# Performance work log

Hardware: AMD Instinct MI355X
Metric: run time of the kernel (lower is better)

## Reference

```python
import jax, jax.numpy as jnp
import numpy as np

RADIUS = 0.1
MAX_GRID_DIM = 96
MAX_COLLISIONS = 128
INCLUDE_SELF = True


def setup_inputs() -> dict:
    key = jax.random.key(0)
    k1, k2, k3 = jax.random.split(key, 3)
    B, N, M, D, C = 2, 8192, 8192, 3, 64
    locs = jax.random.uniform(k1, (B, N, D), dtype=jnp.float32)
    data = jax.random.normal(k2, (B, N, C), dtype=jnp.float32)
    qlocs = jax.random.uniform(k3, (B, M, D), dtype=jnp.float32)
    return {"locs": locs, "data": data, "qlocs": qlocs}


def _hashgrid_order(locs):
    """Returns idxs [B,N] int32 sorting particles by flattened hash-grid cell id.
       idxs[b,i] = original index of the particle at new position i."""
    lower = jnp.min(locs, axis=1, keepdims=True)          # [B,1,D]
    upper = jnp.max(locs, axis=1, keepdims=True)          # [B,1,D]
    # grid dims per batch/dim, cell width = radius, capped at max_grid_dim
    gd = jnp.clip(jnp.floor((upper - lower) / RADIUS).astype(jnp.int32) + 1,
                  1, MAX_GRID_DIM)                        # [B,1,D]
    cell = jnp.floor((locs - lower) / RADIUS).astype(jnp.int32)
    cell = jnp.clip(cell, 0, gd - 1)                      # [B,N,D]
    # mixed-radix flatten: stride[d] = prod(gd[d+1:])
    strides = jnp.concatenate(
        [jnp.cumprod(gd[..., ::-1], axis=-1)[..., ::-1][..., 1:],
         jnp.ones_like(gd[..., :1])], axis=-1)            # [B,1,D]
    cid = jnp.sum(cell * strides, axis=-1)                # [B,N]
    return jnp.argsort(cid, axis=1, stable=True).astype(jnp.int32)


def _collisions(qlocs, nlocs):
    """For each query, indices into reordered locs within RADIUS, lowest-index
       first, padded with -1 up to MAX_COLLISIONS. Returns [B,M,K] int32."""
    B, N, _ = nlocs.shape
    d2 = jnp.sum((qlocs[:, :, None, :] - nlocs[:, None, :, :]) ** 2, axis=-1)  # [B,M,N]
    mask = d2 <= RADIUS * RADIUS
    if not INCLUDE_SELF:
        mask = mask & (d2 > 0)
    # key = particle index if neighbor else N (sentinel); first K after sort
    key = jnp.where(mask, jnp.arange(N, dtype=jnp.int32)[None, None, :], N)
    first_k = jnp.sort(key, axis=-1)[..., :MAX_COLLISIONS]                     # [B,M,K]
    return jnp.where(first_k < N, first_k, -1).astype(jnp.int32)


def reference(locs, data, qlocs):
    idxs = _hashgrid_order(locs)                              # [B,N]
    nlocs = jnp.take_along_axis(locs, idxs[..., None], axis=1)   # reordered locs
    ndata = jnp.take_along_axis(data, idxs[..., None], axis=1)   # reordered data
    neighbors = _collisions(qlocs, nlocs)                     # [B,M,K]
    return nlocs, ndata, idxs, neighbors
```

## Files before the change

### kernel.cpp

```cpp
#include <hip/hip_runtime.h>
#include <cfloat>
#include <math.h>

#define BB 2
#define NN 8192
#define MM 8192
#define CC 64
#define RAD 0.1f
#define R2 0.01f
#define MAXK 128
#define CELL_CAP 4096
#define CS_STRIDE 4100

#define WS_HDR 0
#define WS_SIDX 32
#define WS_CS (WS_SIDX + BB*NN)
#define WS_NL4 (WS_CS + BB*CS_STRIDE)

__device__ __forceinline__ int cell_of(float v, float lo, int g) {
    int c = (int)floorf(__fdiv_rn(v - lo, RAD));
    return min(max(c, 0), g - 1);
}

__global__ __launch_bounds__(1024) void build_kernel(const float* __restrict__ locs,
                                                     int* __restrict__ ws,
                                                     float* __restrict__ idxs_out) {
    const int b = blockIdx.x;
    const int t = threadIdx.x;
    __shared__ int sh[4097 + 1024 + NN];
    int* s_start = sh;
    int* s_aux   = sh + 4097;
    int* s_tmp   = sh + 4097 + 1024;
    float* s_red = (float*)s_tmp;
    __shared__ float s_lo[3];
    __shared__ int   s_g[3];
    __shared__ int   s_str[2];

    const float* L = locs + (size_t)b * NN * 3;

    float mn0 = FLT_MAX, mn1 = FLT_MAX, mn2 = FLT_MAX;
    float mx0 = -FLT_MAX, mx1 = -FLT_MAX, mx2 = -FLT_MAX;
    for (int i = t; i < NN; i += 1024) {
        float x = L[i*3+0], y = L[i*3+1], z = L[i*3+2];
        mn0 = fminf(mn0, x); mx0 = fmaxf(mx0, x);
        mn1 = fminf(mn1, y); mx1 = fmaxf(mx1, y);
        mn2 = fminf(mn2, z); mx2 = fmaxf(mx2, z);
    }
    s_red[t] = mn0; s_red[1024+t] = mn1; s_red[2048+t] = mn2;
    s_red[3072+t] = mx0; s_red[4096+t] = mx1; s_red[5120+t] = mx2;
    __syncthreads();
    for (int s = 512; s > 0; s >>= 1) {
        if (t < s) {
            s_red[t]      = fminf(s_red[t],      s_red[t+s]);
            s_red[1024+t] = fminf(s_red[1024+t], s_red[1024+t+s]);
            s_red[2048+t] = fminf(s_red[2048+t], s_red[2048+t+s]);
            s_red[3072+t] = fmaxf(s_red[3072+t], s_red[3072+t+s]);
            s_red[4096+t] = fmaxf(s_red[4096+t], s_red[4096+t+s]);
            s_red[5120+t] = fmaxf(s_red[5120+t], s_red[5120+t+s]);
        }
        __syncthreads();
    }
    if (t == 0) {
        float lo0 = s_red[0], lo1 = s_red[1024], lo2 = s_red[2048];
        float up0 = s_red[3072], up1 = s_red[4096], up2 = s_red[5120];
        int g0 = min(max((int)floorf(__fdiv_rn(up0 - lo0, RAD)) + 1, 1), 96);
        int g1 = min(max((int)floorf(__fdiv_rn(up1 - lo1, RAD)) + 1, 1), 96);
        int g2 = min(max((int)floorf(__fdiv_rn(up2 - lo2, RAD)) + 1, 1), 96);
        s_lo[0] = lo0; s_lo[1] = lo1; s_lo[2] = lo2;
        s_g[0] = g0; s_g[1] = g1; s_g[2] = g2;
        s_str[0] = g1 * g2; s_str[1] = g2;
        int* hdr = ws + WS_HDR + b * 16;
        hdr[0] = __float_as_int(lo0); hdr[1] = __float_as_int(lo1); hdr[2] = __float_as_int(lo2);
        hdr[3] = g0; hdr[4] = g1; hdr[5] = g2;
        hdr[6] = g1 * g2; hdr[7] = g2; hdr[8] = g0 * g1 * g2;
    }
    __syncthreads();
    const float lo0 = s_lo[0], lo1 = s_lo[1], lo2f = s_lo[2];
    const int g0 = s_g[0], g1 = s_g[1], g2 = s_g[2];
    const int st0 = s_str[0], st1 = s_str[1];
    const int ncells = g0 * g1 * g2;

    for (int c = t; c < CELL_CAP + 1; c += 1024) s_start[c] = 0;
    __syncthreads();

    for (int i = t; i < NN; i += 1024) {
        int c0 = cell_of(L[i*3+0], lo0, g0);
        int c1 = cell_of(L[i*3+1], lo1, g1);
        int c2 = cell_of(L[i*3+2], lo2f, g2);
        atomicAdd(&s_start[c0*st0 + c1*st1 + c2], 1);
    }
    __syncthreads();

    int base4 = t * 4;
    int sum = s_start[base4] + s_start[base4+1] + s_start[base4+2] + s_start[base4+3];
    s_aux[t] = sum;
    __syncthreads();
    for (int off = 1; off < 1024; off <<= 1) {
        int v = (t >= off) ? s_aux[t - off] : 0;
        __syncthreads();
        s_aux[t] += v;
        __syncthreads();
    }
    int run = s_aux[t] - sum;
    for (int k = 0; k < 4; ++k) {
        int cv = s_start[base4 + k];
        s_start[base4 + k] = run;
        run += cv;
    }
    if (t == 1023) s_start[CELL_CAP] = run;
    __syncthreads();

    for (int i = t; i < NN; i += 1024) {
        int c0 = cell_of(L[i*3+0], lo0, g0);
        int c1 = cell_of(L[i*3+1], lo1, g1);
        int c2 = cell_of(L[i*3+2], lo2f, g2);
        int cid = c0*st0 + c1*st1 + c2;
        int pos = atomicAdd(&s_start[cid], 1);
        s_tmp[pos] = i;
    }
    __syncthreads();

    int* cs = ws + WS_CS + b * CS_STRIDE;
    for (int c = t; c <= ncells; c += 1024) cs[c] = (c == 0) ? 0 : s_start[c - 1];

    int* sIdx = ws + WS_SIDX + b * NN;
    for (int p = t; p < NN; p += 1024) {
        int i = s_tmp[p];
        int c0 = cell_of(L[i*3+0], lo0, g0);
        int c1 = cell_of(L[i*3+1], lo1, g1);
        int c2 = cell_of(L[i*3+2], lo2f, g2);
        int cid = c0*st0 + c1*st1 + c2;
        int segs = (cid == 0) ? 0 : s_start[cid - 1];
        int sege = s_start[cid];
        int rank = 0;
        for (int q = segs; q < sege; ++q) rank += (s_tmp[q] < i) ? 1 : 0;
        int f = segs + rank;
        sIdx[f] = i;
        idxs_out[b * NN + f] = (float)i;
    }
}

__global__ __launch_bounds__(256) void reorder_kernel(const float* __restrict__ locs,
                                                      const float* __restrict__ data,
                                                      const int* __restrict__ ws,
                                                      float* __restrict__ nlocs_out,
                                                      float* __restrict__ ndata_out,
                                                      float* __restrict__ nlocs4) {
    int tid = blockIdx.x * 256 + threadIdx.x;
    int b = tid >> 19;
    int r = tid & ((NN * CC) - 1);
    int p = r >> 6;
    int c = r & 63;
    int idx = ws[WS_SIDX + b * NN + p];
    ndata_out[tid] = data[((size_t)b * NN + idx) * CC + c];
    if (c < 3) {
        float v = locs[((size_t)b * NN + idx) * 3 + c];
        nlocs_out[((size_t)b * NN + p) * 3 + c] = v;
        nlocs4[((size_t)b * NN + p) * 4 + c] = v;
    } else if (c == 3) {
        nlocs4[((size_t)b * NN + p) * 4 + 3] = 0.0f;
    }
}

__global__ __launch_bounds__(256) void neigh_kernel(const float* __restrict__ qlocs,
                                                    const float4* __restrict__ P4,
                                                    const int* __restrict__ ws,
                                                    float* __restrict__ neigh_out) {
    const int tid  = blockIdx.x * 256 + threadIdx.x;
    const int q    = tid >> 3;
    const int lane = threadIdx.x & 63;
    const int sub  = lane >> 3;
    const int lg   = lane & 7;
    const int b    = q >> 13;

    const int* hdr = ws + WS_HDR + b * 16;
    float lo0 = __int_as_float(hdr[0]);
    float lo1 = __int_as_float(hdr[1]);
    float lo2f = __int_as_float(hdr[2]);
    int g0 = hdr[3], g1 = hdr[4], g2 = hdr[5];
    int st0 = hdr[6], st1 = hdr[7];
    const int* cs = ws + WS_CS + b * CS_STRIDE;
    const float4* P = P4 + (size_t)b * NN;

    float qx = qlocs[(size_t)q * 3 + 0];
    float qy = qlocs[(size_t)q * 3 + 1];
    float qz = qlocs[(size_t)q * 3 + 2];

    int c0 = (int)floorf(__fdiv_rn(qx - lo0, RAD));
    int c1 = (int)floorf(__fdiv_rn(qy - lo1, RAD));
    int c2 = (int)floorf(__fdiv_rn(qz - lo2f, RAD));
    int a0lo = max(c0 - 1, 0), a0hi = min(c0 + 1, g0 - 1);
    int a1lo = max(c1 - 1, 0), a1hi = min(c1 + 1, g1 - 1);
    int a2lo = max(c2 - 1, 0), a2hi = min(c2 + 1, g2 - 1);

    int cnt = 0;
    float* o = neigh_out + (size_t)q * MAXK;

    if (a0hi >= a0lo && a1hi >= a1lo && a2hi >= a2lo) {
        for (int a0 = a0lo; a0 <= a0hi && cnt < MAXK; ++a0) {
            for (int a1 = a1lo; a1 <= a1hi && cnt < MAXK; ++a1) {
                int basec = a0 * st0 + a1 * st1;
                int ps = cs[basec + a2lo];
                int pe = cs[basec + a2hi + 1];
                for (int base = ps; base < pe && cnt < MAXK; base += 8) {
                    int p = base + lg;
                    bool hit = false;
                    if (p < pe) {
                        float4 v = P[p];
                        float dx = qx - v.x;
                        float dy = qy - v.y;
                        float dz = qz - v.z;
                        float d2 = __fadd_rn(__fadd_rn(__fmul_rn(dx, dx), __fmul_rn(dy, dy)),
                                             __fmul_rn(dz, dz));
                        hit = (d2 <= R2);
                    }
                    unsigned long long m = __ballot(hit);
                    unsigned mb = (unsigned)((m >> (sub * 8)) & 0xFFull);
                    if (hit) {
                        int slot = cnt + __popc(mb & ((1u << lg) - 1u));
                        if (slot < MAXK) o[slot] = (float)p;
                    }
                    cnt += __popc(mb);
                }
            }
        }
    }
    for (int s = cnt + lg; s < MAXK; s += 8) o[s] = -1.0f;
}

extern "C" void kernel_launch(void* const* d_in, const int* in_sizes, int n_in,
                              void* d_out, int out_size, void* d_ws, size_t ws_size,
                              hipStream_t stream) {
    (void)in_sizes; (void)n_in; (void)out_size; (void)ws_size;
    const float* locs  = (const float*)d_in[0];
    const float* data  = (const float*)d_in[1];
    const float* qlocs = (const float*)d_in[2];
    float* out = (float*)d_out;
    float* nlocs_out = out;
    float* ndata_out = out + BB * NN * 3;
    float* idxs_out  = out + BB * NN * 3 + BB * NN * CC;
    float* neigh_out = idxs_out + BB * NN;
    int* wsi = (int*)d_ws;
    float* nlocs4 = (float*)(wsi + WS_NL4);

    build_kernel<<<BB, 1024, 0, stream>>>(locs, wsi, idxs_out);
    reorder_kernel<<<(BB * NN * CC) / 256, 256, 0, stream>>>(locs, data, wsi,
                                                             nlocs_out, ndata_out, nlocs4);
    neigh_kernel<<<(BB * MM * 8) / 256, 256, 0, stream>>>(qlocs, (const float4*)nlocs4, wsi, neigh_out);
}
```

Baseline: 106.8 us.

## Use wave shuffles in build reductions, cache cell ids, widen neighbor query groups

The build kernel now does its min/max reduction and prefix scan with wavefront shuffles instead of long shared-memory tree loops full of block barriers. It also caches each particle's cell id in shared memory so later passes skip recomputing cells from global locs. The neighbor kernel assigns 16 lanes per query instead of 8, preloads all nine cell ranges up front, and drops the early-exit checks on the count. Without those checks, queries that have already filled MAXK slots keep scanning the remaining cells, and each query now occupies twice as many threads.

```diff
diff --git a/kernel.cpp b/kernel.cpp
--- a/kernel.cpp
+++ b/kernel.cpp
@@ -27,11 +27,13 @@
                                                      float* __restrict__ idxs_out) {
     const int b = blockIdx.x;
     const int t = threadIdx.x;
-    __shared__ int sh[4097 + 1024 + NN];
-    int* s_start = sh;
-    int* s_aux   = sh + 4097;
-    int* s_tmp   = sh + 4097 + 1024;
-    float* s_red = (float*)s_tmp;
+    const int lane = t & 63;
+    const int wid = t >> 6;
+    __shared__ int s_start[CELL_CAP + 1];
+    __shared__ int s_aux[16];
+    __shared__ int s_tmp[NN];
+    __shared__ int s_cid[NN];
+    __shared__ float s_red6[16 * 6];
     __shared__ float s_lo[3];
     __shared__ int   s_g[3];
     __shared__ int   s_str[2];
@@ -46,23 +48,30 @@
         mn1 = fminf(mn1, y); mx1 = fmaxf(mx1, y);
         mn2 = fminf(mn2, z); mx2 = fmaxf(mx2, z);
     }
-    s_red[t] = mn0; s_red[1024+t] = mn1; s_red[2048+t] = mn2;
-    s_red[3072+t] = mx0; s_red[4096+t] = mx1; s_red[5120+t] = mx2;
-    __syncthreads();
-    for (int s = 512; s > 0; s >>= 1) {
-        if (t < s) {
-            s_red[t]      = fminf(s_red[t],      s_red[t+s]);
-            s_red[1024+t] = fminf(s_red[1024+t], s_red[1024+t+s]);
-            s_red[2048+t] = fminf(s_red[2048+t], s_red[2048+t+s]);
-            s_red[3072+t] = fmaxf(s_red[3072+t], s_red[3072+t+s]);
-            s_red[4096+t] = fmaxf(s_red[4096+t], s_red[4096+t+s]);
-            s_red[5120+t] = fmaxf(s_red[5120+t], s_red[5120+t+s]);
-        }
-        __syncthreads();
-    }
+    #pragma unroll
+    for (int d = 1; d < 64; d <<= 1) {
+        mn0 = fminf(mn0, __shfl_xor(mn0, d, 64));
+        mn1 = fminf(mn1, __shfl_xor(mn1, d, 64));
+        mn2 = fminf(mn2, __shfl_xor(mn2, d, 64));
+        mx0 = fmaxf(mx0, __shfl_xor(mx0, d, 64));
+        mx1 = fmaxf(mx1, __shfl_xor(mx1, d, 64));
+        mx2 = fmaxf(mx2, __shfl_xor(mx2, d, 64));
+    }
+    if (lane == 0) {
+        s_red6[wid*6+0] = mn0; s_red6[wid*6+1] = mn1; s_red6[wid*6+2] = mn2;
+        s_red6[wid*6+3] = mx0; s_red6[wid*6+4] = mx1; s_red6[wid*6+5] = mx2;
+    }
+    for (int c = t; c < CELL_CAP + 1; c += 1024) s_start[c] = 0;
+    __syncthreads();
     if (t == 0) {
-        float lo0 = s_red[0], lo1 = s_red[1024], lo2 = s_red[2048];
-        float up0 = s_red[3072], up1 = s_red[4096], up2 = s_red[5120];
+        float lo0 = FLT_MAX, lo1 = FLT_MAX, lo2 = FLT_MAX;
+        float up0 = -FLT_MAX, up1 = -FLT_MAX, up2 = -FLT_MAX;
+        for (int w = 0; w < 16; ++w) {
+            lo0 = fminf(lo0, s_red6[w*6+0]); lo1 = fminf(lo1, s_red6[w*6+1]);
+            lo2 = fminf(lo2, s_red6[w*6+2]);
+            up0 = fmaxf(up0, s_red6[w*6+3]); up1 = fmaxf(up1, s_red6[w*6+4]);
+            up2 = fmaxf(up2, s_red6[w*6+5]);
+        }
         int g0 = min(max((int)floorf(__fdiv_rn(up0 - lo0, RAD)) + 1, 1), 96);
         int g1 = min(max((int)floorf(__fdiv_rn(up1 - lo1, RAD)) + 1, 1), 96);
         int g2 = min(max((int)floorf(__fdiv_rn(up2 - lo2, RAD)) + 1, 1), 96);
@@ -80,42 +89,48 @@
     const int st0 = s_str[0], st1 = s_str[1];
     const int ncells = g0 * g1 * g2;
 
-    for (int c = t; c < CELL_CAP + 1; c += 1024) s_start[c] = 0;
-    __syncthreads();
-
-    for (int i = t; i < NN; i += 1024) {
-        int c0 = cell_of(L[i*3+0], lo0, g0);
-        int c1 = cell_of(L[i*3+1], lo1, g1);
-        int c2 = cell_of(L[i*3+2], lo2f, g2);
-        atomicAdd(&s_start[c0*st0 + c1*st1 + c2], 1);
-    }
-    __syncthreads();
-
-    int base4 = t * 4;
-    int sum = s_start[base4] + s_start[base4+1] + s_start[base4+2] + s_start[base4+3];
-    s_aux[t] = sum;
-    __syncthreads();
-    for (int off = 1; off < 1024; off <<= 1) {
-        int v = (t >= off) ? s_aux[t - off] : 0;
-        __syncthreads();
-        s_aux[t] += v;
-        __syncthreads();
-    }
-    int run = s_aux[t] - sum;
-    for (int k = 0; k < 4; ++k) {
-        int cv = s_start[base4 + k];
-        s_start[base4 + k] = run;
-        run += cv;
-    }
-    if (t == 1023) s_start[CELL_CAP] = run;
-    __syncthreads();
-
     for (int i = t; i < NN; i += 1024) {
         int c0 = cell_of(L[i*3+0], lo0, g0);
         int c1 = cell_of(L[i*3+1], lo1, g1);
         int c2 = cell_of(L[i*3+2], lo2f, g2);
         int cid = c0*st0 + c1*st1 + c2;
-        int pos = atomicAdd(&s_start[cid], 1);
+        s_cid[i] = cid;
+        atomicAdd(&s_start[cid], 1);
+    }
+    __syncthreads();
+
+    int base4 = t * 4;
+    int v0 = s_start[base4], v1 = s_start[base4+1], v2 = s_start[base4+2], v3 = s_start[base4+3];
+    int sum = v0 + v1 + v2 + v3;
+    int x = sum;
+    #pragma unroll
+    for (int d = 1; d < 64; d <<= 1) {
+        int v = __shfl_up(x, d, 64);
+        if (lane >= d) x += v;
+    }
+    if (lane == 63) s_aux[wid] = x;
+    __syncthreads();
+    if (wid == 0) {
+        int w = (lane < 16) ? s_aux[lane] : 0;
+        #pragma unroll
+        for (int d = 1; d < 16; d <<= 1) {
+            int v = __shfl_up(w, d, 64);
+            if (lane >= d) w += v;
+        }
+        if (lane < 16) s_aux[lane] = w;
+    }
+    __syncthreads();
+    int waveoff = (wid == 0) ? 0 : s_aux[wid - 1];
+    int run = waveoff + x - sum;
+    s_start[base4]   = run;
+    s_start[base4+1] = run + v0;
+    s_start[base4+2] = run + v0 + v1;
+    s_start[base4+3] = run + v0 + v1 + v2;
+    if (t == 1023) s_start[CELL_CAP] = run + sum;
+    __syncthreads();
+
+    for (int i = t; i < NN; i += 1024) {
+        int pos = atomicAdd(&s_start[s_cid[i]], 1);
         s_tmp[pos] = i;
     }
     __syncthreads();
@@ -126,10 +141,7 @@
     int* sIdx = ws + WS_SIDX + b * NN;
     for (int p = t; p < NN; p += 1024) {
         int i = s_tmp[p];
-        int c0 = cell_of(L[i*3+0], lo0, g0);
-        int c1 = cell_of(L[i*3+1], lo1, g1);
-        int c2 = cell_of(L[i*3+2], lo2f, g2);
-        int cid = c0*st0 + c1*st1 + c2;
+        int cid = s_cid[i];
         int segs = (cid == 0) ? 0 : s_start[cid - 1];
         int sege = s_start[cid];
         int rank = 0;
@@ -167,10 +179,10 @@
                                                     const int* __restrict__ ws,
                                                     float* __restrict__ neigh_out) {
     const int tid  = blockIdx.x * 256 + threadIdx.x;
-    const int q    = tid >> 3;
+    const int q    = tid >> 4;
     const int lane = threadIdx.x & 63;
-    const int sub  = lane >> 3;
-    const int lg   = lane & 7;
+    const int sub  = lane >> 4;
+    const int lg   = lane & 15;
     const int b    = q >> 13;
 
     const int* hdr = ws + WS_HDR + b * 16;
@@ -189,43 +201,51 @@
     int c0 = (int)floorf(__fdiv_rn(qx - lo0, RAD));
     int c1 = (int)floorf(__fdiv_rn(qy - lo1, RAD));
     int c2 = (int)floorf(__fdiv_rn(qz - lo2f, RAD));
-    int a0lo = max(c0 - 1, 0), a0hi = min(c0 + 1, g0 - 1);
-    int a1lo = max(c1 - 1, 0), a1hi = min(c1 + 1, g1 - 1);
     int a2lo = max(c2 - 1, 0), a2hi = min(c2 + 1, g2 - 1);
+    bool zok = (a2lo <= a2hi);
+
+    int rs[9], re[9];
+    #pragma unroll
+    for (int da0 = 0; da0 < 3; ++da0) {
+        #pragma unroll
+        for (int da1 = 0; da1 < 3; ++da1) {
+            int k = da0 * 3 + da1;
+            int a0 = c0 + da0 - 1;
+            int a1 = c1 + da1 - 1;
+            bool ok = zok && (a0 >= 0) && (a0 < g0) && (a1 >= 0) && (a1 < g1);
+            int basec = a0 * st0 + a1 * st1;
+            rs[k] = ok ? cs[basec + a2lo] : 0;
+            re[k] = ok ? cs[basec + a2hi + 1] : 0;
+        }
+    }
 
     int cnt = 0;
     float* o = neigh_out + (size_t)q * MAXK;
-
-    if (a0hi >= a0lo && a1hi >= a1lo && a2hi >= a2lo) {
-        for (int a0 = a0lo; a0 <= a0hi && cnt < MAXK; ++a0) {
-            for (int a1 = a1lo; a1 <= a1hi && cnt < MAXK; ++a1) {
-                int basec = a0 * st0 + a1 * st1;
-                int ps = cs[basec + a2lo];
-                int pe = cs[basec + a2hi + 1];
-                for (int base = ps; base < pe && cnt < MAXK; base += 8) {
-                    int p = base + lg;
-                    bool hit = false;
-                    if (p < pe) {
-                        float4 v = P[p];
-                        float dx = qx - v.x;
-                        float dy = qy - v.y;
-                        float dz = qz - v.z;
-                        float d2 = __fadd_rn(__fadd_rn(__fmul_rn(dx, dx), __fmul_rn(dy, dy)),
-                                             __fmul_rn(dz, dz));
-                        hit = (d2 <= R2);
-                    }
-                    unsigned long long m = __ballot(hit);
-                    unsigned mb = (unsigned)((m >> (sub * 8)) & 0xFFull);
-                    if (hit) {
-                        int slot = cnt + __popc(mb & ((1u << lg) - 1u));
-                        if (slot < MAXK) o[slot] = (float)p;
-                    }
-                    cnt += __popc(mb);
-                }
+    #pragma unroll
+    for (int k = 0; k < 9; ++k) {
+        int ps = rs[k], pe = re[k];
+        for (int base = ps; base < pe; base += 16) {
+            int p = base + lg;
+            bool hit = false;
+            if (p < pe) {
+                float4 v = P[p];
+                float dx = qx - v.x;
+                float dy = qy - v.y;
+                float dz = qz - v.z;
+                float d2 = __fadd_rn(__fadd_rn(__fmul_rn(dx, dx), __fmul_rn(dy, dy)),
+                                     __fmul_rn(dz, dz));
+                hit = (d2 <= R2);
             }
-        }
-    }
-    for (int s = cnt + lg; s < MAXK; s += 8) o[s] = -1.0f;
+            unsigned long long m = __ballot(hit);
+            unsigned mb = (unsigned)((m >> (sub * 16)) & 0xFFFFull);
+            if (hit) {
+                int slot = cnt + __popc(mb & ((1u << lg) - 1u));
+                if (slot < MAXK) o[slot] = (float)p;
+            }
+            cnt += __popc(mb);
+        }
+    }
+    for (int s = cnt + lg; s < MAXK; s += 16) o[s] = -1.0f;
 }
 
 extern "C" void kernel_launch(void* const* d_in, const int* in_sizes, int n_in,
@@ -246,5 +266,5 @@
     build_kernel<<<BB, 1024, 0, stream>>>(locs, wsi, idxs_out);
     reorder_kernel<<<(BB * NN * CC) / 256, 256, 0, stream>>>(locs, data, wsi,
                                                              nlocs_out, ndata_out, nlocs4);
-    neigh_kernel<<<(BB * MM * 8) / 256, 256, 0, stream>>>(qlocs, (const float4*)nlocs4, wsi, neigh_out);
-}
+    neigh_kernel<<<(BB * MM * 16) / 256, 256, 0, stream>>>(qlocs, (const float4*)nlocs4, wsi, neigh_out);
+}
```

After: 94.41 us. 11.6% less time.
